# Kernel optimization log

Hardware: AMD Instinct MI355X
Metric: run time of the kernel (lower is better)

The kernel has to match this reference:

```python
import jax, jax.numpy as jnp
import numpy as np

EPS = 1e-12  # torch F.normalize eps

def l2norm(x, axis):
    n = jnp.sqrt(jnp.sum(x * x, axis=axis, keepdims=True))
    return x / jnp.maximum(n, EPS)

def setup_inputs() -> dict:
    key = jax.random.key(0)
    k1, k2, k3, k4 = jax.random.split(key, 4)
    N, C, H, W, K = 128, 128, 64, 64, 64
    x = jax.random.normal(k1, (N, C, H, W), dtype=jnp.float32)
    conv_w = jax.random.normal(k2, (K, C), dtype=jnp.float32) * 0.1
    conv_b = jax.random.normal(k3, (K,), dtype=jnp.float32) * 0.1
    centroids = jax.random.uniform(k4, (K, C), dtype=jnp.float32)
    return {"x": x, "conv_w": conv_w, "conv_b": conv_b, "centroids": centroids}

def reference(x, conv_w, conv_b, centroids):
    N, C, H, W = x.shape
    K = centroids.shape[0]
    xf = x.reshape(N, C, H * W)               # [N, C, S]
    xf = l2norm(xf, axis=1)                   # normalize_input over channels
    # 1x1 conv -> logits [N, K, S], softmax over clusters
    logits = jnp.einsum('ncs,kc->nks', xf, conv_w) + conv_b[None, :, None]
    a = jax.nn.softmax(logits, axis=1)        # [N, K, S]
    # VLAD: sum_s a[n,k,s]*(x[n,:,s] - c[k]) = (a @ x^T) - (sum_s a) * c
    vlad = jnp.einsum('nks,ncs->nkc', a, xf) - a.sum(axis=-1)[:, :, None] * centroids[None]
    vlad = l2norm(vlad, axis=2)               # intra-normalization
    vlad = vlad.reshape(N, K * C)
    return l2norm(vlad, axis=1)
```

## Files before the change

kernel.cpp:

```cpp
#include <hip/hip_runtime.h>
#include <math.h>

#define N_IMG 128
#define C_DIM 128
#define K_CL  64
#define S_PIX 4096
#define PB    4
#define SPB   (S_PIX/PB)
#define CHK   32
#define NCHK  (SPB/CHK)
#define NBUF  4

typedef __attribute__((ext_vector_type(8))) short bf16x8;
typedef __attribute__((ext_vector_type(4))) float f32x4;

__device__ __forceinline__ unsigned short f2bf_rn(float v) {
    unsigned u = __float_as_uint(v);
    unsigned r = u + 0x7fffu + ((u >> 16) & 1u);
    return (unsigned short)(r >> 16);
}
__device__ __forceinline__ float bf2f(unsigned short h) {
    return __uint_as_float(((unsigned)h) << 16);
}

__device__ __forceinline__ int sx(int c) { return ((c & 3) | ((c & 1) << 2)) & 7; }
__device__ __forceinline__ int sa(int k) { return (k >> 2) & 3; }

__device__ __forceinline__ void cvt8(const float* v, bf16x8& h, bf16x8& l) {
    union { unsigned w[4]; bf16x8 v8; } H, L;
    #pragma unroll
    for (int p = 0; p < 4; ++p) {
        unsigned u0 = __float_as_uint(v[2*p]);
        unsigned u1 = __float_as_uint(v[2*p+1]);
        float r0 = v[2*p]   - __uint_as_float(u0 & 0xffff0000u);
        float r1 = v[2*p+1] - __uint_as_float(u1 & 0xffff0000u);
        H.w[p] = __builtin_amdgcn_perm(u1, u0, 0x07060302u);
        L.w[p] = __builtin_amdgcn_perm(__float_as_uint(r1), __float_as_uint(r0), 0x07060302u);
    }
    h = H.v8; l = L.v8;
}

__device__ __forceinline__ void gll16(const float* g, float* l) {
    __builtin_amdgcn_global_load_lds(
        (const __attribute__((address_space(1))) unsigned int*)(g),
        (__attribute__((address_space(3))) unsigned int*)(l),
        16, 0, 0);
}

__global__ void k_prep(const float* __restrict__ w, unsigned short* __restrict__ wf,
                       float4* __restrict__ out4, float4* __restrict__ asum4) {
    int i = blockIdx.x * 256 + threadIdx.x;
    f32x4 z = (f32x4)0.f;
    if (i < (N_IMG*K_CL*C_DIM)/4) out4[i] = *(float4*)&z;
    if (i < (N_IMG*K_CL)/4)       asum4[i] = *(float4*)&z;
    if (i < 8192) {
        int j = i & 7, l = (i >> 3) & 63, t = (i >> 9) & 3, m = (i >> 11) & 3;
        int k = 16*m + (l & 15);
        int c = 32*t + 4*j + (l >> 4);
        float v = w[k * C_DIM + c];
        unsigned short h = f2bf_rn(v);
        wf[i]        = h;
        wf[8192 + i] = f2bf_rn(v - bf2f(h));
    }
}

__global__ __launch_bounds__(256, 1)
void k_main(const float* __restrict__ x,
            const unsigned short* __restrict__ wf,
            const float* __restrict__ bias,
            float* __restrict__ vlad,
            float* __restrict__ asum)
{
    __shared__ float Xs[NBUF][C_DIM*CHK];
    __shared__ unsigned short aS[2*K_CL*CHK];
    __shared__ __align__(16) float redS[2][2][16];

    const int tid  = threadIdx.x;
    const int lane = tid & 63;
    const int wid  = tid >> 6;
    const int lc   = lane & 15;
    const int g    = lane >> 4;

    const int p  = wid & 1;
    const int mh = wid >> 1;
    const int px = p*16 + lc;
    const int cq = wid * 32;

    const int n  = blockIdx.x / PB;
    const int sp = blockIdx.x % PB;
    const float* xn = x + (size_t)n * (C_DIM * S_PIX) + sp * SPB;

    bf16x8 Wh[2][4], Wl[2][4];
    #pragma unroll
    for (int mm = 0; mm < 2; ++mm)
        #pragma unroll
        for (int t = 0; t < 4; ++t) {
            int m = 2*mh + mm;
            Wh[mm][t] = *(const bf16x8*)&wf[((m*4 + t)*64 + lane)*8];
            Wl[mm][t] = *(const bf16x8*)&wf[((16 + m*4 + t)*64 + lane)*8];
        }
    #pragma unroll
    for (int mm = 0; mm < 2; ++mm)
        #pragma unroll
        for (int t = 0; t < 4; ++t) {
            asm volatile("" : "+v"(Wh[mm][t]));
            asm volatile("" : "+v"(Wl[mm][t]));
        }
    f32x4 bias_r[2];
    #pragma unroll
    for (int mm = 0; mm < 2; ++mm)
        bias_r[mm] = *(const f32x4*)&bias[32*mh + 16*mm + 4*g];

    f32x4 accV[4][2];
    #pragma unroll
    for (int m = 0; m < 4; ++m) { accV[m][0] = (f32x4)0.f; accV[m][1] = (f32x4)0.f; }
    float asum_acc[8];
    #pragma unroll
    for (int i = 0; i < 8; ++i) asum_acc[i] = 0.f;

    const int eA  = g*32 + (((px >> 2) ^ sx(g)) << 2) + (px & 3);
    const int sxB = sx(lc);
    const int saB = sa(lc);
    const int ps  = g >> 1;
    const int sb  = (8*g) & 15;

    auto STAGE = [&](int t, float* Xbuf) {
        #pragma unroll
        for (int i2 = 0; i2 < 4; ++i2) {
            int rowblk = wid*32 + i2*8;
            int row = rowblk + (lane >> 3);
            const float* gp = xn + (size_t)row * S_PIX + t*CHK
                            + 4*((lane & 7) ^ sx(row));
            gll16(gp, &Xbuf[rowblk * 32]);
        }
    };

    STAGE(0, Xs[0]);
    STAGE(1, Xs[1]);
    STAGE(2, Xs[2]);
    asm volatile("s_waitcnt vmcnt(8)" ::: "memory");
    __builtin_amdgcn_s_barrier();
    __builtin_amdgcn_sched_barrier(0);

    for (int ch = 0; ch < NCHK; ++ch) {
        float* Xb = Xs[ch & (NBUF-1)];

        if (ch + 3 < NCHK) STAGE(ch + 3, Xs[(ch + 3) & (NBUF-1)]);

        float s0 = 0.f, s1 = 0.f, s2 = 0.f, s3 = 0.f;
        f32x4 accL[2];
        accL[0] = (f32x4)0.f; accL[1] = (f32x4)0.f;
        #pragma unroll
        for (int t = 0; t < 4; ++t) {
            float xv[8];
            #pragma unroll
            for (int j = 0; j < 8; ++j)
                xv[j] = Xb[eA + 1024*t + 128*j];
            s0 = fmaf(xv[0], xv[0], s0); s1 = fmaf(xv[1], xv[1], s1);
            s2 = fmaf(xv[2], xv[2], s2); s3 = fmaf(xv[3], xv[3], s3);
            s0 = fmaf(xv[4], xv[4], s0); s1 = fmaf(xv[5], xv[5], s1);
            s2 = fmaf(xv[6], xv[6], s2); s3 = fmaf(xv[7], xv[7], s3);
            bf16x8 xh, xl;
            cvt8(xv, xh, xl);
            #pragma unroll
            for (int mm = 0; mm < 2; ++mm) {
                accL[mm] = __builtin_amdgcn_mfma_f32_16x16x32_bf16(Wh[mm][t], xh, accL[mm], 0,0,0);
                accL[mm] = __builtin_amdgcn_mfma_f32_16x16x32_bf16(Wh[mm][t], xl, accL[mm], 0,0,0);
                accL[mm] = __builtin_amdgcn_mfma_f32_16x16x32_bf16(Wl[mm][t], xh, accL[mm], 0,0,0);
            }
        }
        float ss = (s0 + s1) + (s2 + s3);
        ss += __shfl_xor(ss, 16); ss += __shfl_xor(ss, 32);
        float rnorm = 1.0f / fmaxf(sqrtf(ss), 1e-12f);

        float e[8]; float sm = 0.f;
        #pragma unroll
        for (int mm = 0; mm < 2; ++mm)
            #pragma unroll
            for (int jj = 0; jj < 4; ++jj) {
                float t2 = __expf(fmaf(accL[mm][jj], rnorm, bias_r[mm][jj]));
                e[mm*4+jj] = t2;
                sm += t2;
            }
        sm += __shfl_xor(sm, 16); sm += __shfl_xor(sm, 32);
        if (g == 0) redS[p][mh][lc] = sm;

        #pragma unroll
        for (int mm = 0; mm < 2; ++mm)
            #pragma unroll
            for (int jj = 0; jj < 4; ++jj) {
                float ap = e[mm*4+jj] * rnorm;
                unsigned u = __float_as_uint(ap);
                float r = ap - __uint_as_float(u & 0xffff0000u);
                int k  = 32*mh + 16*mm + 4*g + jj;
                int ix = k*32 + (((px >> 3) ^ g) << 3) + (px & 7);
                aS[ix]        = (unsigned short)(u >> 16);
                aS[2048 + ix] = (unsigned short)(__float_as_uint(r) >> 16);
            }

        asm volatile("s_waitcnt lgkmcnt(0)" ::: "memory");
        __builtin_amdgcn_s_barrier();
        __builtin_amdgcn_sched_barrier(0);

        {
            float S = sm + redS[p][mh^1][lc];
            float coef = __builtin_amdgcn_rcpf(S);
            #pragma unroll
            for (int i = 0; i < 8; ++i) asum_acc[i] = fmaf(e[i], coef, asum_acc[i]);
        }

        {
            float4 u0 = *(const float4*)&redS[ps][0][sb];
            float4 u1 = *(const float4*)&redS[ps][0][sb+4];
            float4 v0 = *(const float4*)&redS[ps][1][sb];
            float4 v1 = *(const float4*)&redS[ps][1][sb+4];
            float cf[8] = {u0.x+v0.x, u0.y+v0.y, u0.z+v0.z, u0.w+v0.w,
                           u1.x+v1.x, u1.y+v1.y, u1.z+v1.z, u1.w+v1.w};
            #pragma unroll
            for (int j = 0; j < 8; ++j) cf[j] = __builtin_amdgcn_rcpf(cf[j]);

            bf16x8 Ah[4], Al[4];
            #pragma unroll
            for (int m = 0; m < 4; ++m) {
                int off = (16*m + lc)*32 + ((g ^ saB) << 3);
                Ah[m] = *(const bf16x8*)&aS[off];
                Al[m] = *(const bf16x8*)&aS[2048 + off];
            }
            #pragma unroll
            for (int nn = 0; nn < 2; ++nn) {
                int c  = cq + nn*16 + lc;
                int P0 = (2*g) ^ sxB;
                float4 f0 = *(const float4*)&Xb[c*32 + P0*4];
                float4 f1 = *(const float4*)&Xb[c*32 + (P0 ^ 1)*4];
                float xv[8] = {f0.x*cf[0], f0.y*cf[1], f0.z*cf[2], f0.w*cf[3],
                               f1.x*cf[4], f1.y*cf[5], f1.z*cf[6], f1.w*cf[7]};
                bf16x8 xh, xl;
                cvt8(xv, xh, xl);
                #pragma unroll
                for (int m = 0; m < 4; ++m) {
                    accV[m][nn] = __builtin_amdgcn_mfma_f32_16x16x32_bf16(Ah[m], xh, accV[m][nn], 0,0,0);
                    accV[m][nn] = __builtin_amdgcn_mfma_f32_16x16x32_bf16(Ah[m], xl, accV[m][nn], 0,0,0);
                    accV[m][nn] = __builtin_amdgcn_mfma_f32_16x16x32_bf16(Al[m], xh, accV[m][nn], 0,0,0);
                }
            }
        }

        if (ch + 1 < NCHK) {
            if (ch + 3 < NCHK)
                asm volatile("s_waitcnt vmcnt(8) lgkmcnt(0)" ::: "memory");
            else if (ch + 2 < NCHK)
                asm volatile("s_waitcnt vmcnt(4) lgkmcnt(0)" ::: "memory");
            else
                asm volatile("s_waitcnt vmcnt(0) lgkmcnt(0)" ::: "memory");
            __builtin_amdgcn_s_barrier();
            __builtin_amdgcn_sched_barrier(0);
        }
    }

    float* vb = vlad + (size_t)n * (K_CL * C_DIM);
    #pragma unroll
    for (int m = 0; m < 4; ++m)
        #pragma unroll
        for (int nn = 0; nn < 2; ++nn)
            #pragma unroll
            for (int jj = 0; jj < 4; ++jj)
                atomicAdd(&vb[(16*m + 4*g + jj)*C_DIM + cq + nn*16 + lc],
                          accV[m][nn][jj]);

    #pragma unroll
    for (int i = 0; i < 8; ++i) {
        float v = asum_acc[i];
        v += __shfl_xor(v, 1); v += __shfl_xor(v, 2);
        v += __shfl_xor(v, 4); v += __shfl_xor(v, 8);
        asum_acc[i] = v;
    }
    if (lc == 0) {
        #pragma unroll
        for (int mm = 0; mm < 2; ++mm)
            #pragma unroll
            for (int jj = 0; jj < 4; ++jj)
                atomicAdd(&asum[n*K_CL + 32*mh + 16*mm + 4*g + jj], asum_acc[mm*4+jj]);
    }
}

__global__ __launch_bounds__(256)
void k_final(float* __restrict__ vlad,
             const float* __restrict__ asum,
             const float* __restrict__ cent)
{
    __shared__ float v[K_CL * 132];
    __shared__ float red[K_CL][4];
    __shared__ float rin[K_CL];
    __shared__ float rtot_s;
    const int tid = threadIdx.x;
    const int n   = blockIdx.x;
    float* vb = vlad + (size_t)n * (K_CL * C_DIM);
    const float* as = asum + n * K_CL;

    for (int i = tid; i < K_CL*C_DIM; i += 256) {
        int k = i >> 7, c = i & 127;
        v[k*132 + c] = vb[i] - as[k] * cent[i];
    }
    __syncthreads();
    {
        int k = tid >> 2, p = tid & 3;
        float s2 = 0.f;
        #pragma unroll
        for (int u = 0; u < 32; ++u) { float t = v[k*132 + (u<<2) + p]; s2 = fmaf(t, t, s2); }
        red[k][p] = s2;
    }
    __syncthreads();
    if (tid < K_CL) {
        float s2 = red[tid][0] + red[tid][1] + red[tid][2] + red[tid][3];
        float r  = 1.0f / fmaxf(sqrtf(s2), 1e-12f);
        rin[tid] = r;
        red[tid][0] = s2 * r * r;
    }
    __syncthreads();
    if (tid < 64) {
        float t = red[tid][0];
        t += __shfl_xor(t, 32); t += __shfl_xor(t, 16); t += __shfl_xor(t, 8);
        t += __shfl_xor(t, 4);  t += __shfl_xor(t, 2);  t += __shfl_xor(t, 1);
        if (tid == 0) rtot_s = 1.0f / fmaxf(sqrtf(t), 1e-12f);
    }
    __syncthreads();
    float rt = rtot_s;
    for (int i = tid; i < K_CL*C_DIM; i += 256) {
        vb[i] = v[(i>>7)*132 + (i&127)] * rin[i>>7] * rt;
    }
}

extern "C" void kernel_launch(void* const* d_in, const int* in_sizes, int n_in,
                              void* d_out, int out_size, void* d_ws, size_t ws_size,
                              hipStream_t stream) {
    const float* x    = (const float*)d_in[0];
    const float* w    = (const float*)d_in[1];
    const float* b    = (const float*)d_in[2];
    const float* cent = (const float*)d_in[3];
    float* out = (float*)d_out;
    unsigned short* wf = (unsigned short*)d_ws;
    float* asum = (float*)((char*)d_ws + 32768);

    k_prep<<<(N_IMG*K_CL*C_DIM/4 + 255)/256, 256, 0, stream>>>(
        w, wf, (float4*)out, (float4*)asum);
    k_main<<<N_IMG * PB, 256, 0, stream>>>(x, wf, b, out, asum);
    k_final<<<N_IMG, 256, 0, stream>>>(out, asum, cent);
}
```

Before: 105.3 us.

## Fuse final normalization into main kernel via last-block counter; use exp2

Removes the separate k_final launch. Each image now has an atomic arrival counter, and the last of its PB blocks does the centroid subtraction and both L2 normalizations, reusing the Xs shared buffer. The softmax exponent is also rewritten as exp2f with LOG2E folded into the bias and the norm scale. This saves one kernel launch and its tail, at the cost of extra serial work in the last-arriving block and a threadfence/atomic handshake.

```diff
diff --git a/kernel.cpp b/kernel.cpp
--- a/kernel.cpp
+++ b/kernel.cpp
@@ -48,11 +48,13 @@
 }
 
 __global__ void k_prep(const float* __restrict__ w, unsigned short* __restrict__ wf,
-                       float4* __restrict__ out4, float4* __restrict__ asum4) {
+                       float4* __restrict__ out4, float4* __restrict__ asum4,
+                       int* __restrict__ cnt) {
     int i = blockIdx.x * 256 + threadIdx.x;
     f32x4 z = (f32x4)0.f;
     if (i < (N_IMG*K_CL*C_DIM)/4) out4[i] = *(float4*)&z;
     if (i < (N_IMG*K_CL)/4)       asum4[i] = *(float4*)&z;
+    if (i < N_IMG)                cnt[i] = 0;
     if (i < 8192) {
         int j = i & 7, l = (i >> 3) & 63, t = (i >> 9) & 3, m = (i >> 11) & 3;
         int k = 16*m + (l & 15);
@@ -69,11 +71,16 @@
             const unsigned short* __restrict__ wf,
             const float* __restrict__ bias,
             float* __restrict__ vlad,
-            float* __restrict__ asum)
+            float* __restrict__ asum,
+            const float* __restrict__ cent,
+            int* __restrict__ cnt)
 {
     __shared__ float Xs[NBUF][C_DIM*CHK];
     __shared__ unsigned short aS[2*K_CL*CHK];
     __shared__ __align__(16) float redS[2][2][16];
+    __shared__ int fin_flag;
+    __shared__ float fin_asum[K_CL];
+    __shared__ float rtot_s;
 
     const int tid  = threadIdx.x;
     const int lane = tid & 63;
@@ -90,6 +97,8 @@
     const int sp = blockIdx.x % PB;
     const float* xn = x + (size_t)n * (C_DIM * S_PIX) + sp * SPB;
 
+    const float LOG2E = 1.44269504f;
+
     bf16x8 Wh[2][4], Wl[2][4];
     #pragma unroll
     for (int mm = 0; mm < 2; ++mm)
@@ -108,8 +117,11 @@
         }
     f32x4 bias_r[2];
     #pragma unroll
-    for (int mm = 0; mm < 2; ++mm)
-        bias_r[mm] = *(const f32x4*)&bias[32*mh + 16*mm + 4*g];
+    for (int mm = 0; mm < 2; ++mm) {
+        f32x4 b4 = *(const f32x4*)&bias[32*mh + 16*mm + 4*g];
+        #pragma unroll
+        for (int jj = 0; jj < 4; ++jj) bias_r[mm][jj] = b4[jj] * LOG2E;
+    }
 
     f32x4 accV[4][2];
     #pragma unroll
@@ -172,13 +184,14 @@
         float ss = (s0 + s1) + (s2 + s3);
         ss += __shfl_xor(ss, 16); ss += __shfl_xor(ss, 32);
         float rnorm = 1.0f / fmaxf(sqrtf(ss), 1e-12f);
+        float rn2 = rnorm * LOG2E;
 
         float e[8]; float sm = 0.f;
         #pragma unroll
         for (int mm = 0; mm < 2; ++mm)
             #pragma unroll
             for (int jj = 0; jj < 4; ++jj) {
-                float t2 = __expf(fmaf(accL[mm][jj], rnorm, bias_r[mm][jj]));
+                float t2 = exp2f(fmaf(accL[mm][jj], rn2, bias_r[mm][jj]));
                 e[mm*4+jj] = t2;
                 sm += t2;
             }
@@ -281,47 +294,52 @@
             for (int jj = 0; jj < 4; ++jj)
                 atomicAdd(&asum[n*K_CL + 32*mh + 16*mm + 4*g + jj], asum_acc[mm*4+jj]);
     }
-}
-
-__global__ __launch_bounds__(256)
-void k_final(float* __restrict__ vlad,
-             const float* __restrict__ asum,
-             const float* __restrict__ cent)
-{
-    __shared__ float v[K_CL * 132];
-    __shared__ float red[K_CL][4];
-    __shared__ float rin[K_CL];
-    __shared__ float rtot_s;
-    const int tid = threadIdx.x;
-    const int n   = blockIdx.x;
-    float* vb = vlad + (size_t)n * (K_CL * C_DIM);
-    const float* as = asum + n * K_CL;
-
+
+    __syncthreads();
+    if (tid == 0) {
+        __threadfence();
+        int prev = __hip_atomic_fetch_add(cnt + n, 1, __ATOMIC_ACQ_REL,
+                                          __HIP_MEMORY_SCOPE_AGENT);
+        fin_flag = (prev == PB - 1);
+    }
+    __syncthreads();
+    if (!fin_flag) return;
+
+    float* v    = &Xs[0][0];
+    float* redf = v + K_CL*132;
+    float* rin  = redf + K_CL*4;
+
+    if (tid < K_CL)
+        fin_asum[tid] = __hip_atomic_load(&asum[n*K_CL + tid], __ATOMIC_RELAXED,
+                                          __HIP_MEMORY_SCOPE_AGENT);
+    __syncthreads();
     for (int i = tid; i < K_CL*C_DIM; i += 256) {
         int k = i >> 7, c = i & 127;
-        v[k*132 + c] = vb[i] - as[k] * cent[i];
+        float val = __hip_atomic_load(&vb[i], __ATOMIC_RELAXED,
+                                      __HIP_MEMORY_SCOPE_AGENT);
+        v[k*132 + c] = val - fin_asum[k] * cent[i];
     }
     __syncthreads();
     {
-        int k = tid >> 2, p = tid & 3;
+        int k = tid >> 2, pp = tid & 3;
         float s2 = 0.f;
         #pragma unroll
-        for (int u = 0; u < 32; ++u) { float t = v[k*132 + (u<<2) + p]; s2 = fmaf(t, t, s2); }
-        red[k][p] = s2;
+        for (int u = 0; u < 32; ++u) { float t = v[k*132 + (u<<2) + pp]; s2 = fmaf(t, t, s2); }
+        redf[k*4 + pp] = s2;
     }
     __syncthreads();
     if (tid < K_CL) {
-        float s2 = red[tid][0] + red[tid][1] + red[tid][2] + red[tid][3];
+        float s2 = redf[tid*4+0] + redf[tid*4+1] + redf[tid*4+2] + redf[tid*4+3];
         float r  = 1.0f / fmaxf(sqrtf(s2), 1e-12f);
         rin[tid] = r;
-        red[tid][0] = s2 * r * r;
+        redf[tid*4] = s2 * r * r;
     }
     __syncthreads();
     if (tid < 64) {
-        float t = red[tid][0];
-        t += __shfl_xor(t, 32); t += __shfl_xor(t, 16); t += __shfl_xor(t, 8);
-        t += __shfl_xor(t, 4);  t += __shfl_xor(t, 2);  t += __shfl_xor(t, 1);
-        if (tid == 0) rtot_s = 1.0f / fmaxf(sqrtf(t), 1e-12f);
+        float t2 = redf[tid*4];
+        t2 += __shfl_xor(t2, 32); t2 += __shfl_xor(t2, 16); t2 += __shfl_xor(t2, 8);
+        t2 += __shfl_xor(t2, 4);  t2 += __shfl_xor(t2, 2);  t2 += __shfl_xor(t2, 1);
+        if (tid == 0) rtot_s = 1.0f / fmaxf(sqrtf(t2), 1e-12f);
     }
     __syncthreads();
     float rt = rtot_s;
@@ -340,9 +358,9 @@
     float* out = (float*)d_out;
     unsigned short* wf = (unsigned short*)d_ws;
     float* asum = (float*)((char*)d_ws + 32768);
+    int* cnt    = (int*)((char*)d_ws + 65536);
 
     k_prep<<<(N_IMG*K_CL*C_DIM/4 + 255)/256, 256, 0, stream>>>(
-        w, wf, (float4*)out, (float4*)asum);
-    k_main<<<N_IMG * PB, 256, 0, stream>>>(x, wf, b, out, asum);
-    k_final<<<N_IMG, 256, 0, stream>>>(out, asum, cent);
-}
+        w, wf, (float4*)out, (float4*)asum, cnt);
+    k_main<<<N_IMG * PB, 256, 0, stream>>>(x, wf, b, out, asum, cent, cnt);
+}
```

Result: slower. 136.5 us (+29.7%).
